# Kernel tuning notes

Measured on AMD Instinct MI355X. Metric: run time of the kernel, lower is better.

## Reference

```python
import jax, jax.numpy as jnp
import numpy as np

BETA = 0.25

def _encoder(x, W0, b0, W1, b1, W2, b2):
    # MLP: Linear+ReLU, Linear+ReLU, Linear (dims 768->512->256->64)
    h = jax.nn.relu(x @ W0 + b0)
    h = jax.nn.relu(h @ W1 + b1)
    return h @ W2 + b2

def _rvq(z, codebooks):
    # Residual vector quantization over L=4 levels (structurally distinct loop).
    residual = z
    x_q = jnp.zeros_like(z)
    losses = []
    codes = []
    for l in range(codebooks.shape[0]):
        cb = codebooks[l]  # [K, e]
        # squared L2 distances [N, K] via expansion (avoids materializing [N,K,e])
        d = (jnp.sum(residual * residual, axis=1, keepdims=True)
             - 2.0 * residual @ cb.T
             + jnp.sum(cb * cb, axis=1))
        idx = jnp.argmin(d, axis=1)           # [N]
        q = cb[idx]                            # gather [N, e]
        # codebook loss + beta * commitment loss
        loss = (jnp.mean((jax.lax.stop_gradient(q) - residual) ** 2)
                + BETA * jnp.mean((q - jax.lax.stop_gradient(residual)) ** 2))
        losses.append(loss)
        # straight-through estimator
        q_st = residual + jax.lax.stop_gradient(q - residual)
        residual = residual - q_st
        x_q = x_q + q_st
        codes.append(idx)
    rq_loss = jnp.mean(jnp.stack(losses))
    return x_q, rq_loss, jnp.stack(codes)  # codes: [L, N] int


def setup_inputs() -> dict:
    key = jax.random.key(0)
    ks = jax.random.split(key, 8)
    N, D = 131072, 768
    dims = [768, 512, 256, 64]
    x = jax.random.normal(ks[0], (N, D), dtype=jnp.float32)
    W0 = jax.random.normal(ks[1], (dims[0], dims[1]), dtype=jnp.float32) * (1.0 / np.sqrt(dims[0]))
    b0 = jnp.zeros((dims[1],), dtype=jnp.float32)
    W1 = jax.random.normal(ks[2], (dims[1], dims[2]), dtype=jnp.float32) * (1.0 / np.sqrt(dims[1]))
    b1 = jnp.zeros((dims[2],), dtype=jnp.float32)
    W2 = jax.random.normal(ks[3], (dims[2], dims[3]), dtype=jnp.float32) * (1.0 / np.sqrt(dims[2]))
    b2 = jnp.zeros((dims[3],), dtype=jnp.float32)
    codebooks = jax.random.normal(ks[4], (4, 256, 64), dtype=jnp.float32)
    return {"x": x, "W0": W0, "b0": b0, "W1": W1, "b1": b1, "W2": W2, "b2": b2,
            "codebooks": codebooks}


def reference(x, W0, b0, W1, b1, W2, b2, codebooks):
    z = _encoder(x, W0, b0, W1, b1, W2, b2)          # [N, 64]
    x_q, rq_loss, codes = _rvq(z, codebooks)
    return x_q, rq_loss, codes
```

## Files before the change

### kernel.cpp

```cpp
#include <hip/hip_runtime.h>
#include <hip/hip_bf16.h>


typedef double d2v __attribute__((ext_vector_type(2)));

template<bool RELU, int NCOLSHIFT>
__global__ __launch_bounds__(256) void gemm128(
    const float* __restrict__ A, const float* __restrict__ W,
    const float* __restrict__ bias, float* __restrict__ C,
    int M, int N, int K)
{
    __shared__ float As[2][16][132];
    __shared__ float Bs[2][16][132];

    const int nwg  = gridDim.x;
    const int b    = blockIdx.x;
    const int xcd  = b & 7;
    const int rest = b >> 3;
    const int q8   = nwg >> 3, r8 = nwg & 7;
    const int wg   = (xcd < r8 ? xcd * (q8 + 1) : r8 * (q8 + 1) + (xcd - r8) * q8) + rest;
    const int NCOL = 1 << NCOLSHIFT;

    const int col0 = (wg & (NCOL - 1)) * 128;
    const int row0 = (wg >> NCOLSHIFT) * 128;

    const int tid = threadIdx.x;
    const int tx = tid & 15;
    const int ty = tid >> 4;

    const float* Ab = A + (size_t)row0 * K;
    const float* Wb = W + col0;

    const int am0 = tid >> 2,          ak0 = (tid & 3) * 4;
    const int am1 = (tid + 256) >> 2,  ak1 = ((tid + 256) & 3) * 4;
    const int bk0 = tid >> 5,          bn0 = (tid & 31) * 4;
    const int bk1 = (tid + 256) >> 5,  bn1 = ((tid + 256) & 31) * 4;

    float acc[8][8] = {};

    {
        float4 pa0 = *reinterpret_cast<const float4*>(Ab + (size_t)am0 * K + ak0);
        float4 pa1 = *reinterpret_cast<const float4*>(Ab + (size_t)am1 * K + ak1);
        float4 pb0 = *reinterpret_cast<const float4*>(Wb + (size_t)bk0 * N + bn0);
        float4 pb1 = *reinterpret_cast<const float4*>(Wb + (size_t)bk1 * N + bn1);
        As[0][ak0 + 0][am0] = pa0.x; As[0][ak0 + 1][am0] = pa0.y;
        As[0][ak0 + 2][am0] = pa0.z; As[0][ak0 + 3][am0] = pa0.w;
        As[0][ak1 + 0][am1] = pa1.x; As[0][ak1 + 1][am1] = pa1.y;
        As[0][ak1 + 2][am1] = pa1.z; As[0][ak1 + 3][am1] = pa1.w;
        *reinterpret_cast<float4*>(&Bs[0][bk0][bn0]) = pb0;
        *reinterpret_cast<float4*>(&Bs[0][bk1][bn1]) = pb1;
    }
    __syncthreads();

    int cur = 0;
    for (int k0 = 0; k0 < K; k0 += 16) {
        const bool hasNext = (k0 + 16 < K);
        float4 sa0, sa1, sb0, sb1;
        if (hasNext) {
            const float* An = Ab + k0 + 16;
            const float* Wn = Wb + (size_t)(k0 + 16) * N;
            sa0 = *reinterpret_cast<const float4*>(An + (size_t)am0 * K + ak0);
            sa1 = *reinterpret_cast<const float4*>(An + (size_t)am1 * K + ak1);
            sb0 = *reinterpret_cast<const float4*>(Wn + (size_t)bk0 * N + bn0);
            sb1 = *reinterpret_cast<const float4*>(Wn + (size_t)bk1 * N + bn1);
        }

#pragma unroll
        for (int kk = 0; kk < 16; ++kk) {
            float4 a0 = *reinterpret_cast<const float4*>(&As[cur][kk][ty * 4]);
            float4 a1 = *reinterpret_cast<const float4*>(&As[cur][kk][64 + ty * 4]);
            float4 b0 = *reinterpret_cast<const float4*>(&Bs[cur][kk][tx * 4]);
            float4 b1 = *reinterpret_cast<const float4*>(&Bs[cur][kk][64 + tx * 4]);
            float ar[8] = {a0.x, a0.y, a0.z, a0.w, a1.x, a1.y, a1.z, a1.w};
            float br[8] = {b0.x, b0.y, b0.z, b0.w, b1.x, b1.y, b1.z, b1.w};
#pragma unroll
            for (int m = 0; m < 8; ++m)
#pragma unroll
                for (int n = 0; n < 8; ++n)
                    acc[m][n] = fmaf(ar[m], br[n], acc[m][n]);
        }

        if (hasNext) {
            int nxt = cur ^ 1;
            As[nxt][ak0 + 0][am0] = sa0.x; As[nxt][ak0 + 1][am0] = sa0.y;
            As[nxt][ak0 + 2][am0] = sa0.z; As[nxt][ak0 + 3][am0] = sa0.w;
            As[nxt][ak1 + 0][am1] = sa1.x; As[nxt][ak1 + 1][am1] = sa1.y;
            As[nxt][ak1 + 2][am1] = sa1.z; As[nxt][ak1 + 3][am1] = sa1.w;
            *reinterpret_cast<float4*>(&Bs[nxt][bk0][bn0]) = sb0;
            *reinterpret_cast<float4*>(&Bs[nxt][bk1][bn1]) = sb1;
            __syncthreads();
            cur = nxt;
        }
    }

    float bl[4], bh[4];
#pragma unroll
    for (int n = 0; n < 4; ++n) {
        bl[n] = bias[col0 + tx * 4 + n];
        bh[n] = bias[col0 + 64 + tx * 4 + n];
    }
#pragma unroll
    for (int half = 0; half < 2; ++half) {
#pragma unroll
        for (int r = 0; r < 4; ++r) {
            int m = half * 4 + r;
            int row = row0 + half * 64 + ty * 4 + r;
            float4 lo, hi;
            lo.x = acc[m][0] + bl[0]; lo.y = acc[m][1] + bl[1];
            lo.z = acc[m][2] + bl[2]; lo.w = acc[m][3] + bl[3];
            hi.x = acc[m][4] + bh[0]; hi.y = acc[m][5] + bh[1];
            hi.z = acc[m][6] + bh[2]; hi.w = acc[m][7] + bh[3];
            if (RELU) {
                lo.x = fmaxf(lo.x, 0.f); lo.y = fmaxf(lo.y, 0.f);
                lo.z = fmaxf(lo.z, 0.f); lo.w = fmaxf(lo.w, 0.f);
                hi.x = fmaxf(hi.x, 0.f); hi.y = fmaxf(hi.y, 0.f);
                hi.z = fmaxf(hi.z, 0.f); hi.w = fmaxf(hi.w, 0.f);
            }
            float* Cr = C + (size_t)row * N + col0;
            *reinterpret_cast<float4*>(Cr + tx * 4) = lo;
            *reinterpret_cast<float4*>(Cr + 64 + tx * 4) = hi;
        }
    }
}

template<bool RELU>
__global__ __launch_bounds__(256) void gemm_bias(
    const float* __restrict__ A, const float* __restrict__ W,
    const float* __restrict__ bias, float* __restrict__ C,
    int M, int N, int K)
{
    __shared__ float As[16][132];
    __shared__ float Bs[16][68];

    const int tid = threadIdx.x;
    const int tx = tid & 15;
    const int ty = tid >> 4;
    const int col0 = blockIdx.x * 64;
    const int row0 = blockIdx.y * 128;

    const float* Ab = A + (size_t)row0 * K;
    const float* Wb = W + col0;

    float acc[8][4] = {};

    for (int k0 = 0; k0 < K; k0 += 16) {
#pragma unroll
        for (int i = 0; i < 2; ++i) {
            int pos = tid + i * 256;
            int m  = pos >> 2;
            int k4 = (pos & 3) * 4;
            float4 v = *reinterpret_cast<const float4*>(Ab + (size_t)m * K + k0 + k4);
            As[k4 + 0][m] = v.x; As[k4 + 1][m] = v.y;
            As[k4 + 2][m] = v.z; As[k4 + 3][m] = v.w;
        }
        {
            int kk = tid >> 4;
            int n4 = (tid & 15) * 4;
            float4 v = *reinterpret_cast<const float4*>(Wb + (size_t)(k0 + kk) * N + n4);
            *reinterpret_cast<float4*>(&Bs[kk][n4]) = v;
        }
        __syncthreads();
#pragma unroll
        for (int kk = 0; kk < 16; ++kk) {
            float4 a0 = *reinterpret_cast<const float4*>(&As[kk][ty * 8]);
            float4 a1 = *reinterpret_cast<const float4*>(&As[kk][ty * 8 + 4]);
            float4 bv = *reinterpret_cast<const float4*>(&Bs[kk][tx * 4]);
            float a[8] = {a0.x, a0.y, a0.z, a0.w, a1.x, a1.y, a1.z, a1.w};
            float b[4] = {bv.x, bv.y, bv.z, bv.w};
#pragma unroll
            for (int m = 0; m < 8; ++m)
#pragma unroll
                for (int n = 0; n < 4; ++n)
                    acc[m][n] = fmaf(a[m], b[n], acc[m][n]);
        }
        __syncthreads();
    }

    float bv[4];
#pragma unroll
    for (int n = 0; n < 4; ++n) bv[n] = bias[col0 + tx * 4 + n];
#pragma unroll
    for (int m = 0; m < 8; ++m) {
        int row = row0 + ty * 8 + m;
        float4 o;
        float v0 = acc[m][0] + bv[0];
        float v1 = acc[m][1] + bv[1];
        float v2 = acc[m][2] + bv[2];
        float v3 = acc[m][3] + bv[3];
        if (RELU) {
            v0 = fmaxf(v0, 0.f); v1 = fmaxf(v1, 0.f);
            v2 = fmaxf(v2, 0.f); v3 = fmaxf(v3, 0.f);
        }
        o.x = v0; o.y = v1; o.z = v2; o.w = v3;
        *reinterpret_cast<float4*>(C + (size_t)row * N + col0 + tx * 4) = o;
    }
}

__global__ void cb_norms(const float* __restrict__ cb,
                         double* __restrict__ cn64, float* __restrict__ cnf) {
    int c = blockIdx.x * 64 + threadIdx.x;
    const float* p = cb + (size_t)c * 64;
    double s = 0.0;
#pragma unroll
    for (int j = 0; j < 64; ++j) {
        double v = (double)p[j];
        s = fma(v, v, s);
    }
    cn64[c] = s;
    cnf[c]  = (float)s;
}

__global__ void build_cbw(const float* __restrict__ cb, double* __restrict__ cbw) {
    int i = blockIdx.x * 256 + threadIdx.x;
    cbw[i] = -2.0 * (double)cb[i];
}

#define EGUARD 1e-3

__device__ __forceinline__ double rank64(const double* __restrict__ p,
                                         double R0, const float (&rd)[64]) {
    double c0 = 0.0, c1 = 0.0, c2 = 0.0, c3 = 0.0;
#pragma unroll
    for (int j = 0; j < 16; ++j) {
        d2v x = *reinterpret_cast<const d2v*>(p + j * 4);
        d2v y = *reinterpret_cast<const d2v*>(p + j * 4 + 2);
        c0 = fma(x[0], (double)rd[j * 4 + 0], c0);
        c1 = fma(x[1], (double)rd[j * 4 + 1], c1);
        c2 = fma(y[0], (double)rd[j * 4 + 2], c2);
        c3 = fma(y[1], (double)rd[j * 4 + 3], c3);
    }
    return R0 + ((c0 + c1) + (c2 + c3));
}

__global__ __launch_bounds__(256) void rvq_v5(
    const float* __restrict__ z,
    const float* __restrict__ cbf,
    const double* __restrict__ cbw,
    const double* __restrict__ cn64,
    const float* __restrict__ cnf,
    float* __restrict__ xq,
    float* __restrict__ codes,
    double* __restrict__ partials,
    int row0, int Ntot)
{
    __shared__ float sd1[4][64];
    __shared__ float sd2[4][64];
    __shared__ int   si1[4][64];
    __shared__ int   si2[4][64];

    const int tid  = threadIdx.x;
    const int lane = tid & 63;
    const int w    = tid >> 6;
    const int wu   = __builtin_amdgcn_readfirstlane(w);
    const int blk  = blockIdx.x;
    const int grow0 = row0 + blk * 64;

    float rd[64];
    const float* zr = z + (size_t)(blk * 64 + lane) * 64;
#pragma unroll
    for (int q = 0; q < 16; ++q) {
        float4 v = *reinterpret_cast<const float4*>(zr + q * 4);
        rd[q * 4 + 0] = v.x; rd[q * 4 + 1] = v.y;
        rd[q * 4 + 2] = v.z; rd[q * 4 + 3] = v.w;
    }

    double sse = 0.0;

    for (int lv = 0; lv < 4; ++lv) {
        const int cbase = lv * 256;
        __syncthreads();

        const float* cwl = cbf + (size_t)(cbase + wu * 64) * 64;
        const float* cnl = cnf + cbase + wu * 64;

        float d1 = 3.4e38f, d2 = 3.4e38f;
        int   i1 = 0,       i2 = 0;

#pragma unroll 1
        for (int c = 0; c < 64; ++c) {
            const float* cp = cwl + c * 64;
            float acc8[8];
#pragma unroll
            for (int q = 0; q < 8; ++q) {
                float4 va = *reinterpret_cast<const float4*>(cp + q * 8);
                float4 vb = *reinterpret_cast<const float4*>(cp + q * 8 + 4);
                float t = 0.f;
                t = fmaf(va.x, rd[q * 8 + 0], t);
                t = fmaf(va.y, rd[q * 8 + 1], t);
                t = fmaf(va.z, rd[q * 8 + 2], t);
                t = fmaf(va.w, rd[q * 8 + 3], t);
                t = fmaf(vb.x, rd[q * 8 + 4], t);
                t = fmaf(vb.y, rd[q * 8 + 5], t);
                t = fmaf(vb.z, rd[q * 8 + 6], t);
                t = fmaf(vb.w, rd[q * 8 + 7], t);
                acc8[q] = t;
            }
            float dot = ((acc8[0] + acc8[1]) + (acc8[2] + acc8[3]))
                      + ((acc8[4] + acc8[5]) + (acc8[6] + acc8[7]));
            float d = fmaf(-2.f, dot, cnl[c]);
            int code = wu * 64 + c;
            if (d < d1) { d2 = d1; i2 = i1; d1 = d; i1 = code; }
            else if (d < d2) { d2 = d; i2 = code; }
        }

        sd1[w][lane] = d1; si1[w][lane] = i1;
        sd2[w][lane] = d2; si2[w][lane] = i2;
        __syncthreads();

        float bd1 = sd1[0][lane]; int bi1 = si1[0][lane]; int wstar = 0;
#pragma unroll
        for (int ww = 1; ww < 4; ++ww) {
            float dd = sd1[ww][lane]; int ii = si1[ww][lane];
            if (dd < bd1 || (dd == bd1 && ii < bi1)) { bd1 = dd; bi1 = ii; wstar = ww; }
        }
        float d2g = 3.4e38f; int i2g = 0;
#pragma unroll
        for (int ww = 0; ww < 4; ++ww) {
            float dd = (ww == wstar) ? sd2[ww][lane] : sd1[ww][lane];
            int   ii = (ww == wstar) ? si2[ww][lane] : si1[ww][lane];
            if (dd < d2g) { d2g = dd; i2g = ii; }
        }

        double R1 = rank64(cbw + (size_t)(cbase + bi1) * 64, cn64[cbase + bi1], rd);
        double R2 = rank64(cbw + (size_t)(cbase + i2g) * 64, cn64[cbase + i2g], rd);
        int ci; double Rw;
        if (R1 < R2 || (R1 == R2 && bi1 < i2g)) { ci = bi1; Rw = R1; }
        else                                    { ci = i2g; Rw = R2; }

        if (!(Rw < (double)d2g - EGUARD)) {
            float l8f = fminf(fminf(sd2[0][lane], sd2[1][lane]),
                              fminf(sd2[2][lane], sd2[3][lane]));
            double L8 = (double)l8f;
            double Rm = 1.0e300; int im = 0;
#pragma unroll
            for (int ww = 0; ww < 4; ++ww) {
#pragma unroll
                for (int k = 0; k < 2; ++k) {
                    int cc = k ? si2[ww][lane] : si1[ww][lane];
                    double R = rank64(cbw + (size_t)(cbase + cc) * 64,
                                      cn64[cbase + cc], rd);
                    if (R < Rm || (R == Rm && cc < im)) { Rm = R; im = cc; }
                }
            }
            if (Rm < L8 - EGUARD) {
                ci = im;
            } else {
                double dmin = 1.0e300; int imin = 0;
#pragma unroll 1
                for (int c = 0; c < 256; ++c) {
                    double R = rank64(cbw + (size_t)(cbase + c) * 64,
                                      cn64[cbase + c], rd);
                    if (R < dmin) { dmin = R; imin = c; }
                }
                ci = imin;
            }
        }

        const float* qp = cbf + (size_t)(cbase + ci) * 64;
        double lsse = 0.0;
#pragma unroll
        for (int q = 0; q < 16; ++q) {
            float4 qv = *reinterpret_cast<const float4*>(qp + q * 4);
            float r0 = rd[q * 4 + 0], r1 = rd[q * 4 + 1];
            float r2 = rd[q * 4 + 2], r3 = rd[q * 4 + 3];
            if (w == 0) {
                float e0 = qv.x - r0, e1 = qv.y - r1;
                float e2 = qv.z - r2, e3 = qv.w - r3;
                lsse = fma((double)e0, (double)e0, lsse);
                lsse = fma((double)e1, (double)e1, lsse);
                lsse = fma((double)e2, (double)e2, lsse);
                lsse = fma((double)e3, (double)e3, lsse);
            }
            rd[q * 4 + 0] = r0 - qv.x; rd[q * 4 + 1] = r1 - qv.y;
            rd[q * 4 + 2] = r2 - qv.z; rd[q * 4 + 3] = r3 - qv.w;
        }
        if (w == 0) {
            sse += lsse;
            codes[(size_t)lv * Ntot + grow0 + lane] = (float)ci;
        }
    }

    if (w == 0) {
        size_t base = (size_t)(grow0 + lane) * 64;
#pragma unroll
        for (int q = 0; q < 16; ++q) {
            float4 zv = *reinterpret_cast<const float4*>(zr + q * 4);
            float4 o;
            o.x = zv.x - rd[q * 4 + 0];
            o.y = zv.y - rd[q * 4 + 1];
            o.z = zv.z - rd[q * 4 + 2];
            o.w = zv.w - rd[q * 4 + 3];
            *reinterpret_cast<float4*>(xq + base + q * 4) = o;
        }
        double s = sse;
#pragma unroll
        for (int off = 32; off > 0; off >>= 1) {
            union { double d; int i[2]; } u; u.d = s;
            u.i[0] = __shfl_down(u.i[0], off, 64);
            u.i[1] = __shfl_down(u.i[1], off, 64);
            s += u.d;
        }
        if (lane == 0) partials[grow0 >> 6] = s;
    }
}

__global__ void loss_final(const double* __restrict__ partials, int n,
                           float* __restrict__ out, double scale) {
    __shared__ double s[256];
    double acc = 0.0;
    for (int i = threadIdx.x; i < n; i += 256) acc += partials[i];
    s[threadIdx.x] = acc;
    __syncthreads();
    for (int off = 128; off > 0; off >>= 1) {
        if ((int)threadIdx.x < off) s[threadIdx.x] += s[threadIdx.x + off];
        __syncthreads();
    }
    if (threadIdx.x == 0) *out = (float)(s[0] * scale);
}

extern "C" void kernel_launch(void* const* d_in, const int* in_sizes, int n_in,
                              void* d_out, int out_size, void* d_ws, size_t ws_size,
                              hipStream_t stream) {
    const float* x  = (const float*)d_in[0];
    const float* W0 = (const float*)d_in[1];
    const float* b0 = (const float*)d_in[2];
    const float* W1 = (const float*)d_in[3];
    const float* b1 = (const float*)d_in[4];
    const float* W2 = (const float*)d_in[5];
    const float* b2 = (const float*)d_in[6];
    const float* cb = (const float*)d_in[7];

    const int N = in_sizes[0] / 768;

    float* out   = (float*)d_out;
    float* xq    = out;
    float* loss  = out + (size_t)N * 64;
    float* codes = loss + 1;

    const int nblk_total = N / 64;
    const size_t tail_floats = 131072 + 2048 + 2 * (size_t)nblk_total + 1024 + 64;

    size_t avail = ws_size / 4;
    avail = (avail > tail_floats) ? (avail - tail_floats) : 0;
    int Nc = (int)(avail / 832);
    Nc = (Nc / 128) * 128;
    if (Nc > N) Nc = N;
    if (Nc < 128) Nc = 128;

    float* ws = (float*)d_ws;
    float* h0 = ws;
    float* h1 = h0 + (size_t)Nc * 512;
    float* z  = h1 + (size_t)Nc * 256;
    double* cbw      = (double*)(ws + (size_t)Nc * 832);
    double* cn64     = cbw + 65536;
    double* partials = cn64 + 1024;
    float*  cnf      = (float*)(partials + nblk_total);

    cb_norms <<<16, 64, 0, stream>>>(cb, cn64, cnf);
    build_cbw<<<256, 256, 0, stream>>>(cb, cbw);

    for (int r0 = 0; r0 < N; r0 += Nc) {
        int cur = (N - r0 < Nc) ? (N - r0) : Nc;
        gemm128<true, 2><<<4 * (cur / 128), 256, 0, stream>>>(
            x + (size_t)r0 * 768, W0, b0, h0, cur, 512, 768);
        gemm128<true, 1><<<2 * (cur / 128), 256, 0, stream>>>(
            h0, W1, b1, h1, cur, 256, 512);
        gemm_bias<false><<<dim3(1, cur / 128), 256, 0, stream>>>(
            h1, W2, b2, z, cur, 64, 256);
        rvq_v5<<<cur / 64, 256, 0, stream>>>(
            z, cb, cbw, cn64, cnf, xq, codes, partials, r0, N);
    }

    loss_final<<<1, 256, 0, stream>>>(partials, nblk_total, loss,
                                      1.25 / (4.0 * (double)N * 64.0));
}
```

Before: 2.999 ms.

## Compute RVQ codebook distances with split-bf16 MFMA and keep the residual in LDS

The fp32 scalar FMA distance scan in the RVQ kernel is replaced by bf16 MFMA 16x16x32 instructions. Codebook and residual are each split into high and low bf16 parts and three products are summed to approximate fp32 accuracy. A new kernel builds the codebook in MFMA fragment layout once. The residual moves from per-lane registers into shared memory, and only wave 0 does the fp64 verification and update, with a new fallback full scan when the MFMA distance disagrees with the fp64 rank. The margin is widened, so the fp64 fallback paths may trigger more often.

Measured after the change: 3.340 ms. 11.4% more time.

```diff
diff --git a/kernel.cpp b/kernel.cpp
--- a/kernel.cpp
+++ b/kernel.cpp
@@ -2,7 +2,18 @@
 #include <hip/hip_bf16.h>
 
 
-typedef double d2v __attribute__((ext_vector_type(2)));
+typedef double d2v  __attribute__((ext_vector_type(2)));
+typedef float  f32x4 __attribute__((ext_vector_type(4)));
+typedef short  bf16x8 __attribute__((ext_vector_type(8)));
+
+__device__ __forceinline__ short f2bf(float f) {
+    unsigned u = __float_as_uint(f);
+    unsigned r = (u + 0x7FFFu + ((u >> 16) & 1u)) >> 16;
+    return (short)r;
+}
+__device__ __forceinline__ float bf2f(short s) {
+    return __uint_as_float(((unsigned)(unsigned short)s) << 16);
+}
 
 template<bool RELU, int NCOLSHIFT>
 __global__ __launch_bounds__(256) void gemm128(
@@ -215,34 +226,58 @@
     cbw[i] = -2.0 * (double)cb[i];
 }
 
-#define EGUARD 1e-3
-
-__device__ __forceinline__ double rank64(const double* __restrict__ p,
-                                         double R0, const float (&rd)[64]) {
+__global__ void build_bmf(const float* __restrict__ cb, short* __restrict__ bmf) {
+    int idx = blockIdx.x * 256 + threadIdx.x;
+    int lane = idx & 63;
+    int rest = idx >> 6;
+    int ks   = rest & 1;
+    int part = (rest >> 1) & 1;
+    int ctg  = (rest >> 2) & 15;
+    int lv   = (rest >> 6) & 3;
+    int col = lane & 15, kb = (lane >> 4) * 4;
+    int code = ctg * 16 + col;
+    bf16x8 v;
+#pragma unroll
+    for (int j = 0; j < 8; ++j) {
+        int k = ks * 32 + kb + (j & 3) + 16 * (j >> 2);
+        float u = -2.0f * cb[((size_t)(lv * 256 + code)) * 64 + k];
+        short hb = f2bf(u);
+        v[j] = (part == 0) ? hb : f2bf(u - bf2f(hb));
+    }
+    *reinterpret_cast<bf16x8*>(bmf + (size_t)idx * 8) = v;
+}
+
+#define EGM 6e-3
+
+__device__ __forceinline__ double rank64_l(const double* __restrict__ p,
+                                           double R0, const float* zrow) {
     double c0 = 0.0, c1 = 0.0, c2 = 0.0, c3 = 0.0;
 #pragma unroll
     for (int j = 0; j < 16; ++j) {
         d2v x = *reinterpret_cast<const d2v*>(p + j * 4);
         d2v y = *reinterpret_cast<const d2v*>(p + j * 4 + 2);
-        c0 = fma(x[0], (double)rd[j * 4 + 0], c0);
-        c1 = fma(x[1], (double)rd[j * 4 + 1], c1);
-        c2 = fma(y[0], (double)rd[j * 4 + 2], c2);
-        c3 = fma(y[1], (double)rd[j * 4 + 3], c3);
+        float4 rv = *reinterpret_cast<const float4*>(zrow + j * 4);
+        c0 = fma(x[0], (double)rv.x, c0);
+        c1 = fma(x[1], (double)rv.y, c1);
+        c2 = fma(y[0], (double)rv.z, c2);
+        c3 = fma(y[1], (double)rv.w, c3);
     }
     return R0 + ((c0 + c1) + (c2 + c3));
 }
 
-__global__ __launch_bounds__(256) void rvq_v5(
+__global__ __launch_bounds__(256) void rvq_v8(
     const float* __restrict__ z,
     const float* __restrict__ cbf,
     const double* __restrict__ cbw,
     const double* __restrict__ cn64,
     const float* __restrict__ cnf,
+    const short* __restrict__ bmf,
     float* __restrict__ xq,
     float* __restrict__ codes,
     double* __restrict__ partials,
     int row0, int Ntot)
 {
+    __shared__ float zres[64][68];
     __shared__ float sd1[4][64];
     __shared__ float sd2[4][64];
     __shared__ int   si1[4][64];
@@ -252,145 +287,208 @@
     const int lane = tid & 63;
     const int w    = tid >> 6;
     const int wu   = __builtin_amdgcn_readfirstlane(w);
+    const int l15  = lane & 15;
+    const int lq   = lane >> 4;
+    const int kb   = lq * 4;
     const int blk  = blockIdx.x;
     const int grow0 = row0 + blk * 64;
 
-    float rd[64];
-    const float* zr = z + (size_t)(blk * 64 + lane) * 64;
-#pragma unroll
-    for (int q = 0; q < 16; ++q) {
-        float4 v = *reinterpret_cast<const float4*>(zr + q * 4);
-        rd[q * 4 + 0] = v.x; rd[q * 4 + 1] = v.y;
-        rd[q * 4 + 2] = v.z; rd[q * 4 + 3] = v.w;
-    }
+#pragma unroll
+    for (int i = 0; i < 4; ++i) {
+        int p  = tid + i * 256;
+        int m  = p >> 4;
+        int q4 = (p & 15) * 4;
+        float4 v = *reinterpret_cast<const float4*>(z + (size_t)(blk * 64 + m) * 64 + q4);
+        *reinterpret_cast<float4*>(&zres[m][q4]) = v;
+    }
+    __syncthreads();
 
     double sse = 0.0;
 
     for (int lv = 0; lv < 4; ++lv) {
         const int cbase = lv * 256;
+
+        f32x4 acc[4][4];
+#pragma unroll
+        for (int ct = 0; ct < 4; ++ct) {
+            float c0 = cnf[cbase + (wu * 4 + ct) * 16 + l15];
+#pragma unroll
+            for (int rt = 0; rt < 4; ++rt) {
+                acc[rt][ct][0] = c0; acc[rt][ct][1] = c0;
+                acc[rt][ct][2] = c0; acc[rt][ct][3] = c0;
+            }
+        }
+
+#pragma unroll
+        for (int ks = 0; ks < 2; ++ks) {
+            bf16x8 ah[4], al[4];
+#pragma unroll
+            for (int rt = 0; rt < 4; ++rt) {
+                const float* zp = &zres[rt * 16 + l15][ks * 32 + kb];
+                float4 q0 = *reinterpret_cast<const float4*>(zp);
+                float4 q1 = *reinterpret_cast<const float4*>(zp + 16);
+                float f[8] = {q0.x, q0.y, q0.z, q0.w, q1.x, q1.y, q1.z, q1.w};
+                bf16x8 h, l;
+#pragma unroll
+                for (int j = 0; j < 8; ++j) {
+                    short hb = f2bf(f[j]);
+                    h[j] = hb;
+                    l[j] = f2bf(f[j] - bf2f(hb));
+                }
+                ah[rt] = h; al[rt] = l;
+            }
+            bf16x8 bh[4], bl[4];
+#pragma unroll
+            for (int ct = 0; ct < 4; ++ct) {
+                int ctg = wu * 4 + ct;
+                size_t fh = ((size_t)(lv * 16 + ctg) * 2 + 0) * 2 + ks;
+                size_t fl = ((size_t)(lv * 16 + ctg) * 2 + 1) * 2 + ks;
+                bh[ct] = *reinterpret_cast<const bf16x8*>(bmf + (fh * 64 + lane) * 8);
+                bl[ct] = *reinterpret_cast<const bf16x8*>(bmf + (fl * 64 + lane) * 8);
+            }
+#pragma unroll
+            for (int rt = 0; rt < 4; ++rt)
+#pragma unroll
+                for (int ct = 0; ct < 4; ++ct) {
+                    acc[rt][ct] = __builtin_amdgcn_mfma_f32_16x16x32_bf16(
+                        ah[rt], bh[ct], acc[rt][ct], 0, 0, 0);
+                    acc[rt][ct] = __builtin_amdgcn_mfma_f32_16x16x32_bf16(
+                        al[rt], bh[ct], acc[rt][ct], 0, 0, 0);
+                    acc[rt][ct] = __builtin_amdgcn_mfma_f32_16x16x32_bf16(
+                        ah[rt], bl[ct], acc[rt][ct], 0, 0, 0);
+                }
+        }
+
+#pragma unroll
+        for (int rt = 0; rt < 4; ++rt) {
+#pragma unroll
+            for (int v = 0; v < 4; ++v) {
+                float d1 = acc[rt][0][v]; int i1 = (wu * 4 + 0) * 16 + l15;
+                float d2 = 3.4e38f;       int i2 = i1;
+#pragma unroll
+                for (int ct = 1; ct < 4; ++ct) {
+                    float dd = acc[rt][ct][v]; int ii = (wu * 4 + ct) * 16 + l15;
+                    if (dd < d1 || (dd == d1 && ii < i1)) { d2 = d1; i2 = i1; d1 = dd; i1 = ii; }
+                    else if (dd < d2 || (dd == d2 && ii < i2)) { d2 = dd; i2 = ii; }
+                }
+#pragma unroll
+                for (int m = 1; m < 16; m <<= 1) {
+                    float od1 = __shfl_xor(d1, m, 64); int oi1 = __shfl_xor(i1, m, 64);
+                    float od2 = __shfl_xor(d2, m, 64); int oi2 = __shfl_xor(i2, m, 64);
+                    bool ob = (od1 < d1) || (od1 == d1 && oi1 < i1);
+                    if (ob) {
+                        bool k2 = (d1 < od2) || (d1 == od2 && i1 < oi2);
+                        d2 = k2 ? d1 : od2; i2 = k2 ? i1 : oi2;
+                        d1 = od1; i1 = oi1;
+                    } else {
+                        bool k2 = (od1 < d2) || (od1 == d2 && oi1 < i2);
+                        d2 = k2 ? od1 : d2; i2 = k2 ? oi1 : i2;
+                    }
+                }
+                if (l15 == 0) {
+                    int row = rt * 16 + lq * 4 + v;
+                    sd1[w][row] = d1; si1[w][row] = i1;
+                    sd2[w][row] = d2; si2[w][row] = i2;
+                }
+            }
+        }
         __syncthreads();
 
-        const float* cwl = cbf + (size_t)(cbase + wu * 64) * 64;
-        const float* cnl = cnf + cbase + wu * 64;
-
-        float d1 = 3.4e38f, d2 = 3.4e38f;
-        int   i1 = 0,       i2 = 0;
-
-#pragma unroll 1
-        for (int c = 0; c < 64; ++c) {
-            const float* cp = cwl + c * 64;
-            float acc8[8];
-#pragma unroll
-            for (int q = 0; q < 8; ++q) {
-                float4 va = *reinterpret_cast<const float4*>(cp + q * 8);
-                float4 vb = *reinterpret_cast<const float4*>(cp + q * 8 + 4);
-                float t = 0.f;
-                t = fmaf(va.x, rd[q * 8 + 0], t);
-                t = fmaf(va.y, rd[q * 8 + 1], t);
-                t = fmaf(va.z, rd[q * 8 + 2], t);
-                t = fmaf(va.w, rd[q * 8 + 3], t);
-                t = fmaf(vb.x, rd[q * 8 + 4], t);
-                t = fmaf(vb.y, rd[q * 8 + 5], t);
-                t = fmaf(vb.z, rd[q * 8 + 6], t);
-                t = fmaf(vb.w, rd[q * 8 + 7], t);
-                acc8[q] = t;
-            }
-            float dot = ((acc8[0] + acc8[1]) + (acc8[2] + acc8[3]))
-                      + ((acc8[4] + acc8[5]) + (acc8[6] + acc8[7]));
-            float d = fmaf(-2.f, dot, cnl[c]);
-            int code = wu * 64 + c;
-            if (d < d1) { d2 = d1; i2 = i1; d1 = d; i1 = code; }
-            else if (d < d2) { d2 = d; i2 = code; }
-        }
-
-        sd1[w][lane] = d1; si1[w][lane] = i1;
-        sd2[w][lane] = d2; si2[w][lane] = i2;
-        __syncthreads();
-
-        float bd1 = sd1[0][lane]; int bi1 = si1[0][lane]; int wstar = 0;
-#pragma unroll
-        for (int ww = 1; ww < 4; ++ww) {
-            float dd = sd1[ww][lane]; int ii = si1[ww][lane];
-            if (dd < bd1 || (dd == bd1 && ii < bi1)) { bd1 = dd; bi1 = ii; wstar = ww; }
-        }
-        float d2g = 3.4e38f; int i2g = 0;
-#pragma unroll
-        for (int ww = 0; ww < 4; ++ww) {
-            float dd = (ww == wstar) ? sd2[ww][lane] : sd1[ww][lane];
-            int   ii = (ww == wstar) ? si2[ww][lane] : si1[ww][lane];
-            if (dd < d2g) { d2g = dd; i2g = ii; }
-        }
-
-        double R1 = rank64(cbw + (size_t)(cbase + bi1) * 64, cn64[cbase + bi1], rd);
-        double R2 = rank64(cbw + (size_t)(cbase + i2g) * 64, cn64[cbase + i2g], rd);
-        int ci; double Rw;
-        if (R1 < R2 || (R1 == R2 && bi1 < i2g)) { ci = bi1; Rw = R1; }
-        else                                    { ci = i2g; Rw = R2; }
-
-        if (!(Rw < (double)d2g - EGUARD)) {
-            float l8f = fminf(fminf(sd2[0][lane], sd2[1][lane]),
-                              fminf(sd2[2][lane], sd2[3][lane]));
-            double L8 = (double)l8f;
-            double Rm = 1.0e300; int im = 0;
+        if (w == 0) {
+            const float* zrow = &zres[lane][0];
+            float bd1 = sd1[0][lane]; int bi1 = si1[0][lane]; int wstar = 0;
+#pragma unroll
+            for (int ww = 1; ww < 4; ++ww) {
+                float dd = sd1[ww][lane]; int ii = si1[ww][lane];
+                if (dd < bd1 || (dd == bd1 && ii < bi1)) { bd1 = dd; bi1 = ii; wstar = ww; }
+            }
+            float d2g = 3.4e38f; int i2g = 0;
 #pragma unroll
             for (int ww = 0; ww < 4; ++ww) {
-#pragma unroll
-                for (int k = 0; k < 2; ++k) {
-                    int cc = k ? si2[ww][lane] : si1[ww][lane];
-                    double R = rank64(cbw + (size_t)(cbase + cc) * 64,
-                                      cn64[cbase + cc], rd);
-                    if (R < Rm || (R == Rm && cc < im)) { Rm = R; im = cc; }
-                }
-            }
-            if (Rm < L8 - EGUARD) {
-                ci = im;
-            } else {
+                float dd = (ww == wstar) ? sd2[ww][lane] : sd1[ww][lane];
+                int   ii = (ww == wstar) ? si2[ww][lane] : si1[ww][lane];
+                if (dd < d2g) { d2g = dd; i2g = ii; }
+            }
+
+            double R1 = rank64_l(cbw + (size_t)(cbase + bi1) * 64, cn64[cbase + bi1], zrow);
+            double R2 = rank64_l(cbw + (size_t)(cbase + i2g) * 64, cn64[cbase + i2g], zrow);
+            int ci; double Rw;
+            if (R1 < R2 || (R1 == R2 && bi1 < i2g)) { ci = bi1; Rw = R1; }
+            else                                    { ci = i2g; Rw = R2; }
+
+            bool scan_ok = fabsf(bd1 - (float)R1) <= 0.05f;
+            if (!scan_ok) {
                 double dmin = 1.0e300; int imin = 0;
 #pragma unroll 1
                 for (int c = 0; c < 256; ++c) {
-                    double R = rank64(cbw + (size_t)(cbase + c) * 64,
-                                      cn64[cbase + c], rd);
+                    double R = rank64_l(cbw + (size_t)(cbase + c) * 64,
+                                        cn64[cbase + c], zrow);
                     if (R < dmin) { dmin = R; imin = c; }
                 }
                 ci = imin;
-            }
-        }
-
-        const float* qp = cbf + (size_t)(cbase + ci) * 64;
-        double lsse = 0.0;
-#pragma unroll
-        for (int q = 0; q < 16; ++q) {
-            float4 qv = *reinterpret_cast<const float4*>(qp + q * 4);
-            float r0 = rd[q * 4 + 0], r1 = rd[q * 4 + 1];
-            float r2 = rd[q * 4 + 2], r3 = rd[q * 4 + 3];
-            if (w == 0) {
-                float e0 = qv.x - r0, e1 = qv.y - r1;
-                float e2 = qv.z - r2, e3 = qv.w - r3;
+            } else if (!(Rw < (double)d2g - EGM)) {
+                float l8f = fminf(fminf(sd2[0][lane], sd2[1][lane]),
+                                  fminf(sd2[2][lane], sd2[3][lane]));
+                double L8 = (double)l8f;
+                double Rm = 1.0e300; int im = 0;
+#pragma unroll
+                for (int ww = 0; ww < 4; ++ww) {
+#pragma unroll
+                    for (int k = 0; k < 2; ++k) {
+                        int cc = k ? si2[ww][lane] : si1[ww][lane];
+                        double R = rank64_l(cbw + (size_t)(cbase + cc) * 64,
+                                            cn64[cbase + cc], zrow);
+                        if (R < Rm || (R == Rm && cc < im)) { Rm = R; im = cc; }
+                    }
+                }
+                if (Rm < L8 - EGM) {
+                    ci = im;
+                } else {
+                    double dmin = 1.0e300; int imin = 0;
+#pragma unroll 1
+                    for (int c = 0; c < 256; ++c) {
+                        double R = rank64_l(cbw + (size_t)(cbase + c) * 64,
+                                            cn64[cbase + c], zrow);
+                        if (R < dmin) { dmin = R; imin = c; }
+                    }
+                    ci = imin;
+                }
+            }
+
+            const float* qp = cbf + (size_t)(cbase + ci) * 64;
+            double lsse = 0.0;
+#pragma unroll
+            for (int q4 = 0; q4 < 16; ++q4) {
+                float4 qv = *reinterpret_cast<const float4*>(qp + q4 * 4);
+                float4 rv = *reinterpret_cast<const float4*>(&zres[lane][q4 * 4]);
+                float e0 = qv.x - rv.x, e1 = qv.y - rv.y;
+                float e2 = qv.z - rv.z, e3 = qv.w - rv.w;
                 lsse = fma((double)e0, (double)e0, lsse);
                 lsse = fma((double)e1, (double)e1, lsse);
                 lsse = fma((double)e2, (double)e2, lsse);
                 lsse = fma((double)e3, (double)e3, lsse);
-            }
-            rd[q * 4 + 0] = r0 - qv.x; rd[q * 4 + 1] = r1 - qv.y;
-            rd[q * 4 + 2] = r2 - qv.z; rd[q * 4 + 3] = r3 - qv.w;
-        }
-        if (w == 0) {
+                float4 nv;
+                nv.x = rv.x - qv.x; nv.y = rv.y - qv.y;
+                nv.z = rv.z - qv.z; nv.w = rv.w - qv.w;
+                *reinterpret_cast<float4*>(&zres[lane][q4 * 4]) = nv;
+            }
             sse += lsse;
             codes[(size_t)lv * Ntot + grow0 + lane] = (float)ci;
         }
+        __syncthreads();
     }
 
     if (w == 0) {
+        const float* zr = z + (size_t)(blk * 64 + lane) * 64;
         size_t base = (size_t)(grow0 + lane) * 64;
 #pragma unroll
-        for (int q = 0; q < 16; ++q) {
-            float4 zv = *reinterpret_cast<const float4*>(zr + q * 4);
+        for (int q4 = 0; q4 < 16; ++q4) {
+            float4 zv = *reinterpret_cast<const float4*>(zr + q4 * 4);
+            float4 rv = *reinterpret_cast<const float4*>(&zres[lane][q4 * 4]);
             float4 o;
-            o.x = zv.x - rd[q * 4 + 0];
-            o.y = zv.y - rd[q * 4 + 1];
-            o.z = zv.z - rd[q * 4 + 2];
-            o.w = zv.w - rd[q * 4 + 3];
-            *reinterpret_cast<float4*>(xq + base + q * 4) = o;
+            o.x = zv.x - rv.x; o.y = zv.y - rv.y;
+            o.z = zv.z - rv.z; o.w = zv.w - rv.w;
+            *reinterpret_cast<float4*>(xq + base + q4 * 4) = o;
         }
         double s = sse;
 #pragma unroll
@@ -438,7 +536,8 @@
     float* codes = loss + 1;
 
     const int nblk_total = N / 64;
-    const size_t tail_floats = 131072 + 2048 + 2 * (size_t)nblk_total + 1024 + 64;
+    const size_t tail_floats = 131072 + 2048 + 2 * (size_t)nblk_total + 1024
+                             + 65536 + 64;
 
     size_t avail = ws_size / 4;
     avail = (avail > tail_floats) ? (avail - tail_floats) : 0;
@@ -455,9 +554,11 @@
     double* cn64     = cbw + 65536;
     double* partials = cn64 + 1024;
     float*  cnf      = (float*)(partials + nblk_total);
+    short*  bmf      = (short*)(cnf + 1024);
 
     cb_norms <<<16, 64, 0, stream>>>(cb, cn64, cnf);
     build_cbw<<<256, 256, 0, stream>>>(cb, cbw);
+    build_bmf<<<64, 256, 0, stream>>>(cb, bmf);
 
     for (int r0 = 0; r0 < N; r0 += Nc) {
         int cur = (N - r0 < Nc) ? (N - r0) : Nc;
@@ -467,8 +568,8 @@
             h0, W1, b1, h1, cur, 256, 512);
         gemm_bias<false><<<dim3(1, cur / 128), 256, 0, stream>>>(
             h1, W2, b2, z, cur, 64, 256);
-        rvq_v5<<<cur / 64, 256, 0, stream>>>(
-            z, cb, cbw, cn64, cnf, xq, codes, partials, r0, N);
+        rvq_v8<<<cur / 64, 256, 0, stream>>>(
+            z, cb, cbw, cn64, cnf, bmf, xq, codes, partials, r0, N);
     }
 
     loss_final<<<1, 256, 0, stream>>>(partials, nblk_total, loss,
```
